# Kernel tuning notes

Measured on AMD Instinct MI355X. Metric: run time of the kernel, lower is better.

The kernel has to match this reference:

```python
import jax, jax.numpy as jnp
import numpy as np
from jax import lax

B, ROWS, COLS, K, LATENT = 8, 1536, 16, 32, 16
EPS_REG = 0.01  # torchsort regularization_strength
BIG = 1e30


def setup_inputs() -> dict:
    key = jax.random.key(0)
    ks = jax.random.split(key, 12)
    def w(k, shape):
        return (jax.random.normal(k, shape, jnp.float32) / np.sqrt(shape[0])).astype(jnp.float32)
    return {
        "table": jax.random.uniform(ks[0], (B, ROWS, COLS), jnp.float32),
        "enc_w1": w(ks[1], (COLS, 32)), "enc_b1": 0.01 * jax.random.normal(ks[2], (32,), jnp.float32),
        "enc_w2": w(ks[3], (32, 64)),   "enc_b2": 0.01 * jax.random.normal(ks[4], (64,), jnp.float32),
        "mean_w": w(ks[5], (64, LATENT)), "mean_b": 0.01 * jax.random.normal(ks[6], (LATENT,), jnp.float32),
        "dec_w1": w(ks[7], (LATENT, 32)), "dec_b1": 0.01 * jax.random.normal(ks[8], (32,), jnp.float32),
        "dec_w2": w(ks[9], (32, COLS)),   "dec_b2": 0.01 * jax.random.normal(ks[10], (COLS,), jnp.float32),
        "labels": jax.random.randint(ks[11], (ROWS,), 0, K, jnp.int32),
        "BlockSize": 64,
        "current_epoch": 0,
        "baseline": 0,
    }


def _soft_rank_l2(s, eps):
    # Exact soft_rank (Blondel et al. / torchsort, l2 reg, ascending):
    # project s/eps onto permutahedron of (n,...,1).
    n = s.shape[0]
    x = s / eps
    perm = jnp.argsort(-x)            # descending sort
    xs = x[perm]
    w = jnp.arange(n, 0, -1, dtype=x.dtype)
    # dual = non-increasing isotonic fit of y = xs - w == -iso_inc(-(xs - w))
    y = -(xs - w)
    S = jnp.concatenate([jnp.zeros((1,), x.dtype), jnp.cumsum(y)])
    idx = jnp.arange(n)
    length = jnp.maximum(idx[None, :] - idx[:, None] + 1, 1).astype(x.dtype)
    A = (S[1:][None, :] - S[:n][:, None]) / length           # mean(y[j..k])  [j,k]
    A = jnp.where(idx[None, :] >= idx[:, None], A, BIG)
    Bm = lax.cummin(A, axis=1, reverse=True)                  # min_{k>=i} A[j,k]
    Cm = lax.cummax(Bm, axis=0)                               # max_{j<=i} ...
    iso_inc = jnp.diagonal(Cm)
    dual = -iso_inc
    primal = xs - dual
    inv = jnp.argsort(perm)
    return primal[inv]


def _forward(table, enc_w1, enc_b1, enc_w2, enc_b2, mean_w, mean_b,
             dec_w1, dec_b1, dec_w2, dec_b2, labels, BlockSize):
    b = table.shape[0]
    # VAE (autoencoder path; z = latent mean)
    h = jax.nn.relu(table @ enc_w1 + enc_b1)
    h = jax.nn.relu(h @ enc_w2 + enc_b2)
    z = h @ mean_w + mean_b                                   # [B, rows, 16]
    r = jax.nn.relu(z @ dec_w1 + dec_b1)
    recon = jax.nn.relu(r @ dec_w2 + dec_b2)
    loss = jnp.mean((recon - table) ** 2)
    # clustering scores (labels fixed from batch 0, shared across batch)
    onehot = jax.nn.one_hot(labels, K, dtype=z.dtype)         # [rows, K]
    counts = jnp.maximum(onehot.sum(0), 1.0)                  # [K]
    centers = jnp.einsum('brd,rk->bkd', z, onehot) / counts[None, :, None]
    center_data = centers[:, labels, :]                       # gather back [B, rows, 16]
    d2 = jnp.mean((z - center_data) ** 2, axis=-1)            # [B, rows]
    mn = d2.min(axis=1, keepdims=True); mx = d2.max(axis=1, keepdims=True)
    d2 = (d2 - mn) / (mx - mn)
    scores = d2 + labels.astype(z.dtype)[None, :]
    # training branch
    smn = scores.min(axis=1, keepdims=True); smx = scores.max(axis=1, keepdims=True)
    scaled = (scores - smn) / (smx - smn) * jnp.asarray(b, z.dtype)  # * len(table)
    ranks = jax.vmap(lambda s: _soft_rank_l2(s, EPS_REG))(scaled)
    rank_idx = jnp.argsort(jnp.argsort(scores, axis=1), axis=1) // BlockSize + 1
    rows = table.shape[1]
    return (ranks.reshape(b, rows, 1), rank_idx.reshape(b, rows, 1),
            scores.reshape(b, rows, 1), loss)


def reference(table, enc_w1, enc_b1, enc_w2, enc_b2, mean_w, mean_b,
              dec_w1, dec_b1, dec_w2, dec_b2, labels, BlockSize,
              current_epoch, baseline):
    return _forward(table, enc_w1, enc_b1, enc_w2, enc_b2, mean_w, mean_b,
                    dec_w1, dec_b1, dec_w2, dec_b2, labels, BlockSize)
```

## Files before the change

kernel.cpp:

```cpp
#include <hip/hip_runtime.h>

#define BATCH 8
#define ROWS 1536
#define KCLS 32
#define NTOT (BATCH*ROWS)
#define ELEMS (NTOT*16)
#define SSTRIDE 3073
#define BIGF 1.0e30f

enum : int {
  WS_Z     = 0,
  WS_X     = WS_Z + NTOT*16,
  WS_XS    = WS_X + NTOT,
  WS_S     = WS_XS + NTOT,
  WS_DESC  = WS_S + BATCH*SSTRIDE,
  WS_ASCP  = WS_DESC + NTOT,
  WS_DSCP  = WS_ASCP + 4*NTOT,
  WS_GPART = WS_DSCP + 4*NTOT,
  WS_LOSSP = WS_GPART + BATCH*96*512,
};
#define WS_CPART WS_GPART

#define LW1  0
#define LB1  512
#define LW2  544
#define LB2  2592
#define LMW  2656
#define LMB  3680
#define LDW1 3696
#define LDB1 4208
#define LDW2 4240
#define LDB2 4752
#define LTOT 4768

#define AX   0
#define AH1  16
#define AH2  48
#define AZ   112
#define AR1  128
#define AREC 144
#define ATOT 160
#define ASTRIDE 164

#define RPB 16
#define FWAYS 16

template<int IN_BASE, int IN_N, int OUT_BASE, int OUT_PW, int OUT_TOT,
         int WOFF, int BOFF, bool RELU>
__device__ __forceinline__ void layerw(float* __restrict__ act,
                                       const float* __restrict__ wsh,
                                       int lrow, int fway)
{
  const int o0 = fway * OUT_PW;
  float acc[OUT_PW];
#pragma unroll
  for (int j = 0; j < OUT_PW; ++j) acc[j] = wsh[BOFF + o0 + j];

  const float4* arow = reinterpret_cast<const float4*>(&act[lrow*ASTRIDE + IN_BASE]);
#pragma unroll 2
  for (int i4 = 0; i4 < IN_N/4; ++i4) {
    float4 sv = arow[i4];
    float svx[4];
    svx[0] = sv.x; svx[1] = sv.y; svx[2] = sv.z; svx[3] = sv.w;
#pragma unroll
    for (int u = 0; u < 4; ++u) {
      const float s = svx[u];
      const float* wp = &wsh[WOFF + (i4*4 + u)*OUT_TOT + o0];
      if constexpr (OUT_PW == 1) {
        acc[0] = fmaf(s, wp[0], acc[0]);
      } else if constexpr (OUT_PW == 2) {
        float2 w = *reinterpret_cast<const float2*>(wp);
        acc[0] = fmaf(s, w.x, acc[0]);
        acc[1] = fmaf(s, w.y, acc[1]);
      } else {
#pragma unroll
        for (int q = 0; q < OUT_PW/4; ++q) {
          float4 w = reinterpret_cast<const float4*>(wp)[q];
          acc[q*4+0] = fmaf(s, w.x, acc[q*4+0]);
          acc[q*4+1] = fmaf(s, w.y, acc[q*4+1]);
          acc[q*4+2] = fmaf(s, w.z, acc[q*4+2]);
          acc[q*4+3] = fmaf(s, w.w, acc[q*4+3]);
        }
      }
    }
  }
  float* orow = &act[lrow*ASTRIDE + OUT_BASE + o0];
  if constexpr (OUT_PW == 1) {
    orow[0] = RELU ? fmaxf(acc[0], 0.f) : acc[0];
  } else if constexpr (OUT_PW == 2) {
    float2 v;
    v.x = RELU ? fmaxf(acc[0], 0.f) : acc[0];
    v.y = RELU ? fmaxf(acc[1], 0.f) : acc[1];
    *reinterpret_cast<float2*>(orow) = v;
  } else {
#pragma unroll
    for (int q = 0; q < OUT_PW/4; ++q) {
      float4 v;
      v.x = RELU ? fmaxf(acc[q*4+0], 0.f) : acc[q*4+0];
      v.y = RELU ? fmaxf(acc[q*4+1], 0.f) : acc[q*4+1];
      v.z = RELU ? fmaxf(acc[q*4+2], 0.f) : acc[q*4+2];
      v.w = RELU ? fmaxf(acc[q*4+3], 0.f) : acc[q*4+3];
      reinterpret_cast<float4*>(orow)[q] = v;
    }
  }
}

__global__ __launch_bounds__(256, 4) void k1_ae(
    const float* __restrict__ table,
    const float* __restrict__ w1, const float* __restrict__ b1,
    const float* __restrict__ w2, const float* __restrict__ b2,
    const float* __restrict__ mw, const float* __restrict__ mb,
    const float* __restrict__ dw1, const float* __restrict__ db1,
    const float* __restrict__ dw2, const float* __restrict__ db2,
    const int* __restrict__ labels,
    float* __restrict__ ws)
{
  const int tid  = threadIdx.x;
  const int lrow = tid & (RPB-1);
  const int fway = tid >> 4;
  const int blk  = blockIdx.x;
  const int b    = blk / 96;
  const int ch   = blk % 96;

  __shared__ float wsh[LTOT];
  __shared__ float act[RPB * ASTRIDE];
  __shared__ int   lbl[RPB];
  __shared__ float lred[4];

  {
    float4* d4 = reinterpret_cast<float4*>(wsh);
#define CPY(off, src, nf4) \
    { const float4* p = reinterpret_cast<const float4*>(src); \
      for (int t = tid; t < (nf4); t += 256) d4[(off)/4 + t] = p[t]; }
    CPY(LW1,  w1,  128) CPY(LB1,  b1,  8)  CPY(LW2,  w2,  512)
    CPY(LB2,  b2,  16)  CPY(LMW,  mw,  256) CPY(LMB,  mb,  4)
    CPY(LDW1, dw1, 128) CPY(LDB1, db1, 8)  CPY(LDW2, dw2, 128)
    CPY(LDB2, db2, 4)
#undef CPY
    if (tid < RPB) lbl[tid] = labels[ch * RPB + tid];
    if (tid < RPB*4) {
      const float4 v = reinterpret_cast<const float4*>(table)[blk*(RPB*4) + tid];
      reinterpret_cast<float4*>(act)[(tid >> 2)*(ASTRIDE/4) + (tid & 3)] = v;
    }
  }
  __syncthreads();

  layerw<AX,  16, AH1, 2, 32, LW1,  LB1,  true >(act, wsh, lrow, fway);
  __syncthreads();
  layerw<AH1, 32, AH2, 4, 64, LW2,  LB2,  true >(act, wsh, lrow, fway);
  __syncthreads();
  layerw<AH2, 64, AZ,  1, 16, LMW,  LMB,  false>(act, wsh, lrow, fway);
  __syncthreads();

  if (tid < RPB*4) {
    const float4 zv =
      reinterpret_cast<const float4*>(act)[(tid >> 2)*(ASTRIDE/4) + (AZ/4) + (tid & 3)];
    reinterpret_cast<float4*>(ws + WS_Z)[blk*(RPB*4) + tid] = zv;
  }

  layerw<AZ,  16, AR1, 2, 32, LDW1, LDB1, true >(act, wsh, lrow, fway);
  __syncthreads();
  layerw<AR1, 32, AREC,1, 16, LDW2, LDB2, true >(act, wsh, lrow, fway);
  __syncthreads();

  {
    const float d = act[lrow*ASTRIDE + AREC + fway] - act[lrow*ASTRIDE + AX + fway];
    float ls = d * d;
    for (int off = 32; off > 0; off >>= 1) ls += __shfl_down(ls, off);
    if ((tid & 63) == 0) lred[tid >> 6] = ls;
    __syncthreads();
    if (tid == 0) ws[WS_LOSSP + blk] = (lred[0] + lred[1]) + (lred[2] + lred[3]);
  }

  {
    float a0 = 0.f, a1 = 0.f;
    const int d0 = tid & 15, k0 = tid >> 4;
    const int k1c = k0 + 16;
#pragma unroll
    for (int rr = 0; rr < RPB; ++rr) {
      const int lb = lbl[rr];
      const float zv = act[rr*ASTRIDE + AZ + d0];
      a0 += (lb == k0)  ? zv : 0.f;
      a1 += (lb == k1c) ? zv : 0.f;
    }
    ws[WS_CPART + (b*96 + ch)*512 + tid]       = a0;
    ws[WS_CPART + (b*96 + ch)*512 + 256 + tid] = a1;
  }
}

__global__ __launch_bounds__(256) void k345(const int* __restrict__ labels,
                                            float* __restrict__ ws,
                                            float* __restrict__ out)
{
  const int b = blockIdx.x;
  const int tid = threadIdx.x;
  __shared__ int cnt[KCLS];
  __shared__ float cent[512];
  __shared__ float rmn[256], rmx[256];
  __shared__ int lbl_l[ROWS];

  rmn[tid] = ws[WS_LOSSP + tid] + ws[WS_LOSSP + 256 + tid] + ws[WS_LOSSP + 512 + tid];
  if (tid < KCLS) cnt[tid] = 0;
  __syncthreads();
  for (int off = 128; off > 0; off >>= 1) {
    if (tid < off) rmn[tid] += rmn[tid + off];
    __syncthreads();
  }
  if (b == 0 && tid == 0) out[3*NTOT] = rmn[0] / (float)ELEMS;

#pragma unroll
  for (int c = 0; c < 6; ++c) {
    int lb = labels[c*256 + tid];
    lbl_l[c*256 + tid] = lb;
    atomicAdd(&cnt[lb], 1);
  }
  __syncthreads();
#pragma unroll
  for (int e = tid; e < 512; e += 256) {
    float s = 0.f;
    for (int c = 0; c < 96; ++c) s += ws[WS_CPART + (b*96 + c)*512 + e];
    const int cn = cnt[e >> 4] > 1 ? cnt[e >> 4] : 1;
    cent[e] = s / (float)cn;
  }
  __syncthreads();

  float d2v[6];
  float tmn = 3.0e38f, tmx = -3.0e38f;
#pragma unroll
  for (int c = 0; c < 6; ++c) {
    const int r = c*256 + tid;
    const int lb = lbl_l[r];
    const float4* zp = reinterpret_cast<const float4*>(ws + WS_Z + (b*ROWS + r)*16);
    const float4* cp = reinterpret_cast<const float4*>(&cent[lb*16]);
    float s = 0.f;
#pragma unroll
    for (int q = 0; q < 4; ++q) {
      float4 zv = zp[q], cv = cp[q];
      float d0 = zv.x - cv.x, d1 = zv.y - cv.y, d2_ = zv.z - cv.z, d3 = zv.w - cv.w;
      s += d0*d0 + d1*d1 + d2_*d2_ + d3*d3;
    }
    d2v[c] = s / 16.f;
    tmn = fminf(tmn, d2v[c]); tmx = fmaxf(tmx, d2v[c]);
  }
  rmn[tid] = tmn; rmx[tid] = tmx;
  __syncthreads();
  for (int off = 128; off > 0; off >>= 1) {
    if (tid < off) {
      rmn[tid] = fminf(rmn[tid], rmn[tid + off]);
      rmx[tid] = fmaxf(rmx[tid], rmx[tid + off]);
    }
    __syncthreads();
  }
  const float mn = rmn[0], mx = rmx[0];
  __syncthreads();

  float sv[6];
  tmn = 3.0e38f; tmx = -3.0e38f;
#pragma unroll
  for (int c = 0; c < 6; ++c) {
    const int r = c*256 + tid;
    float sc = (d2v[c] - mn) / (mx - mn) + (float)lbl_l[r];
    sv[c] = sc;
    out[2*NTOT + b*ROWS + r] = sc;
    tmn = fminf(tmn, sc); tmx = fmaxf(tmx, sc);
  }
  rmn[tid] = tmn; rmx[tid] = tmx;
  __syncthreads();
  for (int off = 128; off > 0; off >>= 1) {
    if (tid < off) {
      rmn[tid] = fminf(rmn[tid], rmn[tid + off]);
      rmx[tid] = fmaxf(rmx[tid], rmx[tid + off]);
    }
    __syncthreads();
  }
  const float smn = rmn[0], smx = rmx[0];
#pragma unroll
  for (int c = 0; c < 6; ++c) {
    const int r = c*256 + tid;
    float scl = (sv[c] - smn) / (smx - smn) * 8.0f;
    ws[WS_X + b*ROWS + r] = scl / 0.01f;
  }
}

__global__ __launch_bounds__(256) void k6_count(float* __restrict__ ws,
                                                const float* __restrict__ out)
{
  const int bi = blockIdx.x;
  const int jb = bi & 3, rb = (bi >> 2) % 6, b = bi / 24;
  const int tid = threadIdx.x;
  __shared__ float4 sld[96], xld[96];
  {
    float* sf = reinterpret_cast<float*>(sld);
    float* xf = reinterpret_cast<float*>(xld);
    const int base = b*ROWS + jb*384;
    sf[tid] = out[2*NTOT + base + tid];
    xf[tid] = ws[WS_X + base + tid];
    if (tid < 128) {
      sf[256 + tid] = out[2*NTOT + base + 256 + tid];
      xf[256 + tid] = ws[WS_X + base + 256 + tid];
    }
  }
  __syncthreads();
  const int r = rb*256 + tid;
  const float si = out[2*NTOT + b*ROWS + r];
  const float xi = ws[WS_X + b*ROWS + r];
  int asc = 0, dsc = 0;
  const int j0 = jb*384;
#pragma unroll 4
  for (int kk = 0; kk < 96; ++kk) {
    const float4 s4 = sld[kk];
    const float4 x4 = xld[kk];
    const int j = j0 + kk*4;
    asc += (s4.x < si || (s4.x == si && j   < r)) ? 1 : 0;
    asc += (s4.y < si || (s4.y == si && j+1 < r)) ? 1 : 0;
    asc += (s4.z < si || (s4.z == si && j+2 < r)) ? 1 : 0;
    asc += (s4.w < si || (s4.w == si && j+3 < r)) ? 1 : 0;
    dsc += (x4.x > xi || (x4.x == xi && j   < r)) ? 1 : 0;
    dsc += (x4.y > xi || (x4.y == xi && j+1 < r)) ? 1 : 0;
    dsc += (x4.z > xi || (x4.z == xi && j+2 < r)) ? 1 : 0;
    dsc += (x4.w > xi || (x4.w == xi && j+3 < r)) ? 1 : 0;
  }
  int* wsi = reinterpret_cast<int*>(ws);
  wsi[WS_ASCP + jb*NTOT + b*ROWS + r] = asc;
  wsi[WS_DSCP + jb*NTOT + b*ROWS + r] = dsc;
}

__global__ __launch_bounds__(256) void k67(const int* __restrict__ bsp,
                                           float* __restrict__ ws,
                                           float* __restrict__ out)
{
  const int b = blockIdx.x, tid = threadIdx.x;
  __shared__ float xs_l[ROWS];
  __shared__ float ts[256];
  const int* wsi = reinterpret_cast<const int*>(ws);
  int* wsw = reinterpret_cast<int*>(ws);
  const int BS = *bsp;
#pragma unroll
  for (int c = 0; c < 6; ++c) {
    const int r = c*256 + tid;
    const int idx = b*ROWS + r;
    int asc = 0, dsc = 0;
#pragma unroll
    for (int jb = 0; jb < 4; ++jb) {
      asc += wsi[WS_ASCP + jb*NTOT + idx];
      dsc += wsi[WS_DSCP + jb*NTOT + idx];
    }
    out[NTOT + idx] = (float)(asc / BS + 1);
    wsw[WS_DESC + idx] = dsc;
    xs_l[dsc] = ws[WS_X + idx];
  }
  __syncthreads();
  const int base = tid * 6;
  float y[6], sum = 0.f;
#pragma unroll
  for (int u = 0; u < 6; ++u) {
    ws[WS_XS + b*ROWS + base + u] = xs_l[base + u];
    y[u] = (float)(ROWS - (base + u)) - xs_l[base + u];
    sum += y[u];
  }
  ts[tid] = sum;
  __syncthreads();
  for (int off = 1; off < 256; off <<= 1) {
    float v = ts[tid];
    if (tid >= off) v += ts[tid - off];
    __syncthreads();
    ts[tid] = v;
    __syncthreads();
  }
  float run = tid ? ts[tid - 1] : 0.f;
  float* S = ws + WS_S + b*SSTRIDE;
#pragma unroll
  for (int u = 0; u < 6; ++u) { S[base + u] = run; run += y[u]; }
  if (tid == 255) S[ROWS] = run;
#pragma unroll
  for (int u = 0; u < 6; ++u) S[ROWS + 1 + tid*6 + u] = BIGF;
}

__global__ __launch_bounds__(256) void k8a(float* __restrict__ ws)
{
  const int bi = blockIdx.x;
  const int c = bi & 7, ib = (bi >> 3) % 6, b = bi / 48;
  const int tid = threadIdx.x;
  __shared__ float Sseg[448];
  __shared__ float invl[192];
  const float* S = ws + WS_S + b*SSTRIDE;
  const int ibase = ib*256;
  const int segbase = ibase + c*192 + 1;
  Sseg[tid] = S[segbase + tid];
  if (tid < 192) {
    Sseg[256 + tid] = S[segbase + 256 + tid];
    invl[tid] = 1.0f / (float)(c*192 + tid + 1);
  }
  __syncthreads();
  const int i = ibase + tid;
  const float Si = S[i];
  float gm = 3.0e38f;
#pragma unroll 8
  for (int k = 0; k < 192; ++k)
    gm = fminf(gm, (Sseg[tid + k] - Si) * invl[k]);
  ws[WS_GPART + (b*8 + c)*ROWS + i] = gm;
}

__global__ __launch_bounds__(768) void k8b(float* __restrict__ ws,
                                           float* __restrict__ out)
{
  const int b = blockIdx.x, tid = threadIdx.x;
  __shared__ float g[ROWS];
  __shared__ float pm[768];
  for (int t = tid; t < ROWS; t += 768) {
    float gm = 3.0e38f;
#pragma unroll
    for (int c = 0; c < 8; ++c)
      gm = fminf(gm, ws[WS_GPART + (b*8 + c)*ROWS + t]);
    g[t] = gm;
  }
  __syncthreads();
  const float a = g[2*tid], cc = g[2*tid + 1];
  pm[tid] = fmaxf(a, cc);
  __syncthreads();
  for (int off = 1; off < 768; off <<= 1) {
    float v = pm[tid];
    if (tid >= off) v = fmaxf(v, pm[tid - off]);
    __syncthreads();
    pm[tid] = v;
    __syncthreads();
  }
  const float excl = tid ? pm[tid - 1] : -3.0e38f;
  const float i0 = fmaxf(excl, a);
  const float i1 = fmaxf(i0, cc);
  g[2*tid] = i0; g[2*tid + 1] = i1;
  __syncthreads();
  const float* xs = ws + WS_XS + b*ROWS;
  const int* desc = reinterpret_cast<const int*>(ws) + WS_DESC + b*ROWS;
  for (int t = tid; t < ROWS; t += 768) {
    const int dr = desc[t];
    out[b*ROWS + t] = xs[dr] + g[dr];
  }
}

extern "C" void kernel_launch(void* const* d_in, const int* in_sizes, int n_in,
                              void* d_out, int out_size, void* d_ws, size_t ws_size,
                              hipStream_t stream) {
  const float* table = (const float*)d_in[0];
  const float* w1  = (const float*)d_in[1];
  const float* b1  = (const float*)d_in[2];
  const float* w2  = (const float*)d_in[3];
  const float* b2  = (const float*)d_in[4];
  const float* mw  = (const float*)d_in[5];
  const float* mb  = (const float*)d_in[6];
  const float* dw1 = (const float*)d_in[7];
  const float* db1 = (const float*)d_in[8];
  const float* dw2 = (const float*)d_in[9];
  const float* db2 = (const float*)d_in[10];
  const int* labels = (const int*)d_in[11];
  const int* bsp    = (const int*)d_in[12];
  float* out = (float*)d_out;
  float* ws  = (float*)d_ws;

  k1_ae<<<768, 256, 0, stream>>>(table, w1, b1, w2, b2, mw, mb, dw1, db1, dw2, db2, labels, ws);
  k345<<<8, 256, 0, stream>>>(labels, ws, out);
  k6_count<<<192, 256, 0, stream>>>(ws, out);
  k67<<<8, 256, 0, stream>>>(bsp, ws, out);
  k8a<<<384, 256, 0, stream>>>(ws);
  k8b<<<8, 768, 0, stream>>>(ws, out);
}
```

Before: 66.26 us.

## Fuse score computation into rank-count kernel and use wave-shuffle scans

Merges the per-batch score/normalisation kernel into the rank-counting kernel. Each of the 24 blocks per batch recomputes the centroids, distances and scaled scores redundantly, then counts ranks directly from shared memory, which removes one launch and a global round trip. The shared-memory Hillis-Steele prefix scans in k67 and k8b are replaced with wavefront shuffle scans plus a per-wave totals pass, cutting the number of barriers. The cost is 24x redundant centroid reduction work (each block reads the 96x512 centroid partials) and more shared memory per block.

```diff
diff --git a/kernel.cpp b/kernel.cpp
--- a/kernel.cpp
+++ b/kernel.cpp
@@ -39,11 +39,9 @@
 #define AZ   112
 #define AR1  128
 #define AREC 144
-#define ATOT 160
 #define ASTRIDE 164
 
 #define RPB 16
-#define FWAYS 16
 
 template<int IN_BASE, int IN_N, int OUT_BASE, int OUT_PW, int OUT_TOT,
          int WOFF, int BOFF, bool RELU>
@@ -188,33 +186,41 @@
   }
 }
 
-__global__ __launch_bounds__(256) void k345(const int* __restrict__ labels,
+__global__ __launch_bounds__(256) void kmid(const int* __restrict__ labels,
                                             float* __restrict__ ws,
                                             float* __restrict__ out)
 {
-  const int b = blockIdx.x;
+  const int bi = blockIdx.x;
+  const int jb = bi & 3, rb = (bi >> 2) % 6, b = bi / 24;
   const int tid = threadIdx.x;
-  __shared__ int cnt[KCLS];
+
+  __shared__ int   cnt[KCLS];
+  __shared__ int   lbl_l[ROWS];
   __shared__ float cent[512];
+  alignas(16) __shared__ float s_l[ROWS];
+  alignas(16) __shared__ float d2x[ROWS];
   __shared__ float rmn[256], rmx[256];
-  __shared__ int lbl_l[ROWS];
-
-  rmn[tid] = ws[WS_LOSSP + tid] + ws[WS_LOSSP + 256 + tid] + ws[WS_LOSSP + 512 + tid];
+
   if (tid < KCLS) cnt[tid] = 0;
-  __syncthreads();
-  for (int off = 128; off > 0; off >>= 1) {
-    if (tid < off) rmn[tid] += rmn[tid + off];
-    __syncthreads();
-  }
-  if (b == 0 && tid == 0) out[3*NTOT] = rmn[0] / (float)ELEMS;
-
+  if (bi == 0) {
+    rmn[tid] = ws[WS_LOSSP + tid] + ws[WS_LOSSP + 256 + tid] + ws[WS_LOSSP + 512 + tid];
+  }
+  __syncthreads();
 #pragma unroll
   for (int c = 0; c < 6; ++c) {
-    int lb = labels[c*256 + tid];
+    const int lb = labels[c*256 + tid];
     lbl_l[c*256 + tid] = lb;
     atomicAdd(&cnt[lb], 1);
   }
-  __syncthreads();
+  if (bi == 0) {
+    for (int off = 128; off > 0; off >>= 1) {
+      __syncthreads();
+      if (tid < off) rmn[tid] += rmn[tid + off];
+    }
+    if (tid == 0) out[3*NTOT] = rmn[0] / (float)ELEMS;
+  }
+  __syncthreads();
+
 #pragma unroll
   for (int e = tid; e < 512; e += 256) {
     float s = 0.f;
@@ -224,7 +230,6 @@
   }
   __syncthreads();
 
-  float d2v[6];
   float tmn = 3.0e38f, tmx = -3.0e38f;
 #pragma unroll
   for (int c = 0; c < 6; ++c) {
@@ -239,8 +244,9 @@
       float d0 = zv.x - cv.x, d1 = zv.y - cv.y, d2_ = zv.z - cv.z, d3 = zv.w - cv.w;
       s += d0*d0 + d1*d1 + d2_*d2_ + d3*d3;
     }
-    d2v[c] = s / 16.f;
-    tmn = fminf(tmn, d2v[c]); tmx = fmaxf(tmx, d2v[c]);
+    const float dv = s / 16.f;
+    d2x[r] = dv;
+    tmn = fminf(tmn, dv); tmx = fmaxf(tmx, dv);
   }
   rmn[tid] = tmn; rmx[tid] = tmx;
   __syncthreads();
@@ -254,14 +260,13 @@
   const float mn = rmn[0], mx = rmx[0];
   __syncthreads();
 
-  float sv[6];
   tmn = 3.0e38f; tmx = -3.0e38f;
 #pragma unroll
   for (int c = 0; c < 6; ++c) {
     const int r = c*256 + tid;
-    float sc = (d2v[c] - mn) / (mx - mn) + (float)lbl_l[r];
-    sv[c] = sc;
-    out[2*NTOT + b*ROWS + r] = sc;
+    const float sc = (d2x[r] - mn) / (mx - mn) + (float)lbl_l[r];
+    s_l[r] = sc;
+    if (jb == 0 && c == rb) out[2*NTOT + b*ROWS + r] = sc;
     tmn = fminf(tmn, sc); tmx = fmaxf(tmx, sc);
   }
   rmn[tid] = tmn; rmx[tid] = tmx;
@@ -274,55 +279,41 @@
     __syncthreads();
   }
   const float smn = rmn[0], smx = rmx[0];
+  __syncthreads();
+
 #pragma unroll
   for (int c = 0; c < 6; ++c) {
     const int r = c*256 + tid;
-    float scl = (sv[c] - smn) / (smx - smn) * 8.0f;
-    ws[WS_X + b*ROWS + r] = scl / 0.01f;
-  }
-}
-
-__global__ __launch_bounds__(256) void k6_count(float* __restrict__ ws,
-                                                const float* __restrict__ out)
-{
-  const int bi = blockIdx.x;
-  const int jb = bi & 3, rb = (bi >> 2) % 6, b = bi / 24;
-  const int tid = threadIdx.x;
-  __shared__ float4 sld[96], xld[96];
-  {
-    float* sf = reinterpret_cast<float*>(sld);
-    float* xf = reinterpret_cast<float*>(xld);
-    const int base = b*ROWS + jb*384;
-    sf[tid] = out[2*NTOT + base + tid];
-    xf[tid] = ws[WS_X + base + tid];
-    if (tid < 128) {
-      sf[256 + tid] = out[2*NTOT + base + 256 + tid];
-      xf[256 + tid] = ws[WS_X + base + 256 + tid];
-    }
-  }
-  __syncthreads();
-  const int r = rb*256 + tid;
-  const float si = out[2*NTOT + b*ROWS + r];
-  const float xi = ws[WS_X + b*ROWS + r];
+    const float scl = (s_l[r] - smn) / (smx - smn) * 8.0f;
+    const float xv = scl / 0.01f;
+    d2x[r] = xv;
+    if (jb == 0 && c == rb) ws[WS_X + b*ROWS + r] = xv;
+  }
+  __syncthreads();
+
+  const int r0 = rb*256 + tid;
+  const float si = s_l[r0], xi = d2x[r0];
   int asc = 0, dsc = 0;
   const int j0 = jb*384;
+  const float4* s4p = reinterpret_cast<const float4*>(&s_l[j0]);
+  const float4* x4p = reinterpret_cast<const float4*>(&d2x[j0]);
 #pragma unroll 4
   for (int kk = 0; kk < 96; ++kk) {
-    const float4 s4 = sld[kk];
-    const float4 x4 = xld[kk];
+    const float4 s4 = s4p[kk];
+    const float4 x4 = x4p[kk];
     const int j = j0 + kk*4;
-    asc += (s4.x < si || (s4.x == si && j   < r)) ? 1 : 0;
-    asc += (s4.y < si || (s4.y == si && j+1 < r)) ? 1 : 0;
-    asc += (s4.z < si || (s4.z == si && j+2 < r)) ? 1 : 0;
-    asc += (s4.w < si || (s4.w == si && j+3 < r)) ? 1 : 0;
-    dsc += (x4.x > xi || (x4.x == xi && j   < r)) ? 1 : 0;
-    dsc += (x4.y > xi || (x4.y == xi && j+1 < r)) ? 1 : 0;
-    dsc += (x4.z > xi || (x4.z == xi && j+2 < r)) ? 1 : 0;
-    dsc += (x4.w > xi || (x4.w == xi && j+3 < r)) ? 1 : 0;
+    asc += (s4.x < si || (s4.x == si && j   < r0)) ? 1 : 0;
+    asc += (s4.y < si || (s4.y == si && j+1 < r0)) ? 1 : 0;
+    asc += (s4.z < si || (s4.z == si && j+2 < r0)) ? 1 : 0;
+    asc += (s4.w < si || (s4.w == si && j+3 < r0)) ? 1 : 0;
+    dsc += (x4.x > xi || (x4.x == xi && j   < r0)) ? 1 : 0;
+    dsc += (x4.y > xi || (x4.y == xi && j+1 < r0)) ? 1 : 0;
+    dsc += (x4.z > xi || (x4.z == xi && j+2 < r0)) ? 1 : 0;
+    dsc += (x4.w > xi || (x4.w == xi && j+3 < r0)) ? 1 : 0;
   }
   int* wsi = reinterpret_cast<int*>(ws);
-  wsi[WS_ASCP + jb*NTOT + b*ROWS + r] = asc;
-  wsi[WS_DSCP + jb*NTOT + b*ROWS + r] = dsc;
+  wsi[WS_ASCP + jb*NTOT + b*ROWS + r0] = asc;
+  wsi[WS_DSCP + jb*NTOT + b*ROWS + r0] = dsc;
 }
 
 __global__ __launch_bounds__(256) void k67(const int* __restrict__ bsp,
@@ -330,8 +321,9 @@
                                            float* __restrict__ out)
 {
   const int b = blockIdx.x, tid = threadIdx.x;
+  const int lane = tid & 63, wav = tid >> 6;
   __shared__ float xs_l[ROWS];
-  __shared__ float ts[256];
+  __shared__ float wtot[4];
   const int* wsi = reinterpret_cast<const int*>(ws);
   int* wsw = reinterpret_cast<int*>(ws);
   const int BS = *bsp;
@@ -351,23 +343,24 @@
   }
   __syncthreads();
   const int base = tid * 6;
-  float y[6], sum = 0.f;
+  float y[6], own = 0.f;
 #pragma unroll
   for (int u = 0; u < 6; ++u) {
     ws[WS_XS + b*ROWS + base + u] = xs_l[base + u];
     y[u] = (float)(ROWS - (base + u)) - xs_l[base + u];
-    sum += y[u];
-  }
-  ts[tid] = sum;
-  __syncthreads();
-  for (int off = 1; off < 256; off <<= 1) {
-    float v = ts[tid];
-    if (tid >= off) v += ts[tid - off];
-    __syncthreads();
-    ts[tid] = v;
-    __syncthreads();
-  }
-  float run = tid ? ts[tid - 1] : 0.f;
+    own += y[u];
+  }
+  float v = own;
+#pragma unroll
+  for (int d = 1; d < 64; d <<= 1) {
+    float o = __shfl_up(v, d);
+    if (lane >= d) v += o;
+  }
+  if (lane == 63) wtot[wav] = v;
+  __syncthreads();
+  float wpre = 0.f;
+  for (int w = 0; w < wav; ++w) wpre += wtot[w];
+  float run = wpre + (v - own);
   float* S = ws + WS_S + b*SSTRIDE;
 #pragma unroll
   for (int u = 0; u < 6; ++u) { S[base + u] = run; run += y[u]; }
@@ -405,8 +398,9 @@
                                            float* __restrict__ out)
 {
   const int b = blockIdx.x, tid = threadIdx.x;
+  const int lane = tid & 63, wav = tid >> 6;
   __shared__ float g[ROWS];
-  __shared__ float pm[768];
+  __shared__ float wtot[12];
   for (int t = tid; t < ROWS; t += 768) {
     float gm = 3.0e38f;
 #pragma unroll
@@ -416,16 +410,19 @@
   }
   __syncthreads();
   const float a = g[2*tid], cc = g[2*tid + 1];
-  pm[tid] = fmaxf(a, cc);
-  __syncthreads();
-  for (int off = 1; off < 768; off <<= 1) {
-    float v = pm[tid];
-    if (tid >= off) v = fmaxf(v, pm[tid - off]);
-    __syncthreads();
-    pm[tid] = v;
-    __syncthreads();
-  }
-  const float excl = tid ? pm[tid - 1] : -3.0e38f;
+  float v = fmaxf(a, cc);
+#pragma unroll
+  for (int d = 1; d < 64; d <<= 1) {
+    float o = __shfl_up(v, d);
+    if (lane >= d) v = fmaxf(v, o);
+  }
+  if (lane == 63) wtot[wav] = v;
+  __syncthreads();
+  float wpre = -3.0e38f;
+  for (int w = 0; w < wav; ++w) wpre = fmaxf(wpre, wtot[w]);
+  float lex = __shfl_up(v, 1);
+  if (lane == 0) lex = -3.0e38f;
+  const float excl = fmaxf(wpre, lex);
   const float i0 = fmaxf(excl, a);
   const float i1 = fmaxf(i0, cc);
   g[2*tid] = i0; g[2*tid + 1] = i1;
@@ -458,8 +455,7 @@
   float* ws  = (float*)d_ws;
 
   k1_ae<<<768, 256, 0, stream>>>(table, w1, b1, w2, b2, mw, mb, dw1, db1, dw2, db2, labels, ws);
-  k345<<<8, 256, 0, stream>>>(labels, ws, out);
-  k6_count<<<192, 256, 0, stream>>>(ws, out);
+  kmid<<<192, 256, 0, stream>>>(labels, ws, out);
   k67<<<8, 256, 0, stream>>>(bsp, ws, out);
   k8a<<<384, 256, 0, stream>>>(ws);
   k8b<<<8, 768, 0, stream>>>(ws, out);
```

After: 66.00 us. About the same (-0.4%).
